# Kernel optimization log

Hardware: AMD Instinct MI355X
Metric: run time of the kernel (lower is better)

Reference implementation:

```python
import jax, jax.numpy as jnp
import numpy as np

D_GNN, D_MODEL = 512, 2048
B, T = 4, 4096
EPS = 1e-5


def layer_norm(x, gamma, beta):
    mu = jnp.mean(x, axis=-1, keepdims=True)
    var = jnp.mean(jnp.square(x - mu), axis=-1, keepdims=True)
    return (x - mu) * jax.lax.rsqrt(var + EPS) * gamma + beta


def setup_inputs() -> dict:
    key = jax.random.key(0)
    ks = jax.random.split(key, 10)
    s_proj = 1.0 / np.sqrt(D_GNN)
    s_mod = 1.0 / np.sqrt(D_MODEL)
    s_gate = 1.0 / np.sqrt(2 * D_MODEL)
    return {
        "h_llm": jax.random.normal(ks[0], (B, T, D_MODEL), jnp.float32),
        "h_change": jax.random.normal(ks[1], (B, D_GNN), jnp.float32),
        # h_change_proj: Linear(d_gnn -> d_model)
        "w_proj": jax.random.uniform(ks[2], (D_MODEL, D_GNN), jnp.float32, -s_proj, s_proj),
        "b_proj": jnp.zeros((D_MODEL,), jnp.float32),
        "g1": jnp.ones((D_MODEL,), jnp.float32),
        "b1": jnp.zeros((D_MODEL,), jnp.float32),
        # MHA value / output projections (q,k are mathematically irrelevant: kv_len==1 -> softmax==1)
        "w_v": jax.random.uniform(ks[3], (D_MODEL, D_MODEL), jnp.float32, -s_mod, s_mod),
        "b_v": jnp.zeros((D_MODEL,), jnp.float32),
        "w_o": jax.random.uniform(ks[4], (D_MODEL, D_MODEL), jnp.float32, -s_mod, s_mod),
        "b_o": jnp.zeros((D_MODEL,), jnp.float32),
        "g2": jnp.ones((D_MODEL,), jnp.float32),
        "b2": jnp.zeros((D_MODEL,), jnp.float32),
        # fusion gate: Linear(2*d_model -> d_model) + sigmoid
        "w_gate": jax.random.uniform(ks[5], (D_MODEL, 2 * D_MODEL), jnp.float32, -s_gate, s_gate),
        "b_gate": jnp.zeros((D_MODEL,), jnp.float32),
        "g3": jnp.ones((D_MODEL,), jnp.float32),
        "b3": jnp.zeros((D_MODEL,), jnp.float32),
    }


def reference(h_llm, h_change, w_proj, b_proj, g1, b1, w_v, b_v, w_o, b_o,
              g2, b2, w_gate, b_gate, g3, b3):
    # project GNN feature to d_model, then LayerNorm  -> (B, D)
    hc = layer_norm(h_change @ w_proj.T + b_proj, g1, b1)
    # cross-attention with kv_len == 1: softmax over a single key is identically 1,
    # so attn_output == out_proj(value_proj(hc)), broadcast over T. Dropout is eval (identity).
    attn = (hc @ w_v.T + b_v) @ w_o.T + b_o                 # (B, D)
    attn_out = layer_norm(h_llm + attn[:, None, :], g2, b2)  # (B, T, D)
    # gated residual fusion: gate = sigmoid(W [h_llm ; attn_out] + b)
    wg_l, wg_a = w_gate[:, :D_MODEL], w_gate[:, D_MODEL:]
    gate = jax.nn.sigmoid(h_llm @ wg_l.T + attn_out @ wg_a.T + b_gate)
    fused = gate * attn_out + (1.0 - gate) * h_llm
    return layer_norm(fused, g3, b3)
```

## Files before the change

kernel.cpp:

```cpp
#include <hip/hip_runtime.h>
#include <hip/hip_bf16.h>
#include <cstdint>
#include <cstddef>

#define DM 2048
#define DG 512
#define NBATCH 4
#define NT 4096
#define NM (NBATCH*NT)
#define KC (2*DM)
#define LN_EPS 1e-5f
#define NTILES (KC/128)
#define SCL_A 16.0f
#define SCL_B 8192.0f
#define DESCALE (1.0f/131072.0f)

typedef __bf16 bf16;
typedef bf16 bf16x8 __attribute__((ext_vector_type(8)));
typedef float f32x4 __attribute__((ext_vector_type(4)));
typedef int   i32x4 __attribute__((ext_vector_type(4)));
typedef char  i8x8  __attribute__((ext_vector_type(8)));

#define AS1 __attribute__((address_space(1)))
#define AS3 __attribute__((address_space(3)))

__device__ __forceinline__ char q8(float x, float s) {
    int v = (int)rintf(x * s);
    v = v > 127 ? 127 : (v < -127 ? -127 : v);
    return (char)v;
}

__device__ __forceinline__ void block_reduce_2(float& s, float& s2) {
#pragma unroll
    for (int off = 32; off; off >>= 1) {
        s  += __shfl_down(s, off);
        s2 += __shfl_down(s2, off);
    }
    __shared__ float sm[8];
    const int wid = threadIdx.x >> 6, lane = threadIdx.x & 63;
    if (lane == 0) { sm[wid] = s; sm[4 + wid] = s2; }
    __syncthreads();
    s  = sm[0] + sm[1] + sm[2] + sm[3];
    s2 = sm[4] + sm[5] + sm[6] + sm[7];
}

__global__ void k_cvt_i8(const float* __restrict__ src, int8_t* __restrict__ dst, int n8) {
    int i = blockIdx.x * blockDim.x + threadIdx.x;
    if (i >= n8) return;
    const f32x4* s = (const f32x4*)src + (size_t)i * 2;
    f32x4 a = s[0], b = s[1];
    i8x8 o;
#pragma unroll
    for (int q = 0; q < 4; q++) { o[q] = q8(a[q], SCL_B); o[4+q] = q8(b[q], SCL_B); }
    *((i8x8*)dst + i) = o;
}

template<int K>
__global__ void k_dot(const float* __restrict__ X, const float* __restrict__ W,
                      const float* __restrict__ bias, float* __restrict__ out) {
    const int lane = threadIdx.x & 63;
    const int wid  = threadIdx.x >> 6;
    const int j = blockIdx.x * 4 + wid;
    const f32x4* Wr = (const f32x4*)(W + (size_t)j * K);
    float acc[NBATCH] = {0.f, 0.f, 0.f, 0.f};
    constexpr int C = K / 4 / 64;
#pragma unroll
    for (int i = 0; i < C; i++) {
        f32x4 wv = Wr[lane + 64 * i];
#pragma unroll
        for (int b = 0; b < NBATCH; b++) {
            f32x4 xv = ((const f32x4*)(X + (size_t)b * K))[lane + 64 * i];
            acc[b] += wv[0]*xv[0] + wv[1]*xv[1] + wv[2]*xv[2] + wv[3]*xv[3];
        }
    }
#pragma unroll
    for (int off = 32; off; off >>= 1)
#pragma unroll
        for (int b = 0; b < NBATCH; b++) acc[b] += __shfl_down(acc[b], off);
    if (lane == 0) {
        const float bb = bias[j];
#pragma unroll
        for (int b = 0; b < NBATCH; b++) out[(size_t)b * DM + j] = acc[b] + bb;
    }
}

__global__ void k_ln_small(const float* __restrict__ in, const float* __restrict__ g,
                           const float* __restrict__ bt, float* __restrict__ out) {
    const int row = blockIdx.x;
    const int tid = threadIdx.x;
    const f32x4* ir = (const f32x4*)(in + (size_t)row * DM);
    f32x4 v0 = ir[tid], v1 = ir[tid + 256];
    float s  = v0[0]+v0[1]+v0[2]+v0[3] + v1[0]+v1[1]+v1[2]+v1[3];
    float s2 = v0[0]*v0[0]+v0[1]*v0[1]+v0[2]*v0[2]+v0[3]*v0[3]
             + v1[0]*v1[0]+v1[1]*v1[1]+v1[2]*v1[2]+v1[3]*v1[3];
    block_reduce_2(s, s2);
    const float mu = s * (1.0f / DM);
    const float r  = rsqrtf(s2 * (1.0f / DM) - mu * mu + LN_EPS);
    f32x4 g0 = ((const f32x4*)g)[tid],  g1v = ((const f32x4*)g)[tid + 256];
    f32x4 b0 = ((const f32x4*)bt)[tid], b1v = ((const f32x4*)bt)[tid + 256];
    f32x4 o0 = (v0 - mu) * r * g0 + b0;
    f32x4 o1 = (v1 - mu) * r * g1v + b1v;
    f32x4* orow = (f32x4*)(out + (size_t)row * DM);
    orow[tid] = o0; orow[tid + 256] = o1;
}

__global__ void k_stats_pack(const float* __restrict__ h, const float* __restrict__ attnv,
                             const float* __restrict__ g2, const float* __restrict__ b2,
                             int8_t* __restrict__ Aq, bf16* __restrict__ hbf,
                             float* __restrict__ muA, float* __restrict__ rA) {
    const int m = blockIdx.x;
    const int b = m >> 12;
    const int tid = threadIdx.x;
    const f32x4* hr = (const f32x4*)(h + (size_t)m * DM);
    const f32x4* ar = (const f32x4*)(attnv + (size_t)b * DM);
    f32x4 h0 = hr[2*tid], h1 = hr[2*tid + 1];
    f32x4 a0 = ar[2*tid], a1 = ar[2*tid + 1];
    f32x4 x0 = h0 + a0, x1 = h1 + a1;
    float s  = x0[0]+x0[1]+x0[2]+x0[3] + x1[0]+x1[1]+x1[2]+x1[3];
    float s2 = x0[0]*x0[0]+x0[1]*x0[1]+x0[2]*x0[2]+x0[3]*x0[3]
             + x1[0]*x1[0]+x1[1]*x1[1]+x1[2]*x1[2]+x1[3]*x1[3];
    block_reduce_2(s, s2);
    const float mu = s * (1.0f / DM);
    const float r  = rsqrtf(s2 * (1.0f / DM) - mu * mu + LN_EPS);
    if (tid == 0) { muA[m] = mu; rA[m] = r; }
    f32x4 gg0 = ((const f32x4*)g2)[2*tid], gg1 = ((const f32x4*)g2)[2*tid + 1];
    f32x4 bb0 = ((const f32x4*)b2)[2*tid], bb1 = ((const f32x4*)b2)[2*tid + 1];
    f32x4 ao0 = (x0 - mu) * r * gg0 + bb0;
    f32x4 ao1 = (x1 - mu) * r * gg1 + bb1;
    bf16x8 hv;
#pragma unroll
    for (int q = 0; q < 4; q++) { hv[q] = (bf16)h0[q]; hv[4+q] = (bf16)h1[q]; }
    *(bf16x8*)(hbf + (size_t)m * DM + 8*tid) = hv;
    i8x8 qh, qa;
#pragma unroll
    for (int q = 0; q < 4; q++) {
        qh[q] = q8(h0[q], SCL_A);  qh[4+q] = q8(h1[q], SCL_A);
        qa[q] = q8(ao0[q], SCL_A); qa[4+q] = q8(ao1[q], SCL_A);
    }
    *(i8x8*)(Aq + (size_t)m * KC + 8*tid) = qh;
    *(i8x8*)(Aq + (size_t)m * KC + DM + 8*tid) = qa;
}

#define MF(a,b,c) __builtin_amdgcn_mfma_i32_16x16x64_i8(a,b,c,0,0,0)
#define SCHED0() __builtin_amdgcn_sched_barrier(0)
#define BAR()  { SCHED0(); asm volatile("s_barrier" ::: "memory"); SCHED0(); }
#define VM(n)  { asm volatile("s_waitcnt vmcnt(" #n ")" ::: "memory"); SCHED0(); }
#define LGKM(n) { asm volatile("s_waitcnt lgkmcnt(" #n ")" ::: "memory"); SCHED0(); }

__global__ __launch_bounds__(512, 2) void k_gemm256(const int8_t* __restrict__ A, const int8_t* __restrict__ Bw,
                                                    const float* __restrict__ bgate, bf16* __restrict__ gl) {
    __shared__ __align__(128) char smem[131072];
    const int tid  = threadIdx.x;
    const int lane = tid & 63;
    const int wid  = tid >> 6;
    const int wm   = wid >> 2, wn = wid & 3;

    const int swz = (blockIdx.x & 7) * 64 + (blockIdx.x >> 3);
    const int bm = (swz >> 3) << 8;
    const int bn = (swz & 7) << 8;

    const int r_local = tid >> 3;
    const int sc = (tid & 7) ^ (r_local & 7);
    const int8_t* Abase = A  + (size_t)(bm + r_local) * KC + sc*16;
    const int8_t* Bbase = Bw + (size_t)(bn + r_local) * KC + sc*16;
    const int ldsW = wid << 10;

#define STAGEA(buf, rnd, kt) __builtin_amdgcn_global_load_lds( \
        (const AS1 void*)(Abase + (size_t)(rnd)*64*KC + (kt)*128), \
        (AS3 void*)(smem + (buf)*65536 + (rnd)*8192 + ldsW), 16, 0, 0)
#define STAGEB(buf, rnd, kt) __builtin_amdgcn_global_load_lds( \
        (const AS1 void*)(Bbase + (size_t)(rnd)*64*KC + (kt)*128), \
        (AS3 void*)(smem + (buf)*65536 + 32768 + (rnd)*8192 + ldsW), 16, 0, 0)

    const int co0 = ((lane >> 4) ^ (lane & 7)) << 4;
    const int co1 = ((4 + (lane >> 4)) ^ (lane & 7)) << 4;
    const int arowb = (wm*128 + (lane & 15)) * 128;
    const int browb = (wn*64  + (lane & 15)) * 128;

#define AFRG(buf, m, ks) (*(const i32x4*)(smem + (buf)*65536 + arowb + (m)*2048 + ((ks) ? co1 : co0)))
#define BFRG(buf, n, ks) (*(const i32x4*)(smem + (buf)*65536 + 32768 + browb + (n)*2048 + ((ks) ? co1 : co0)))

    i32x4 acc[8][4] = {};
    i32x4 aLo[4][2], aHi[4][2], b01[2][2], b23[2][2];

#define LOAD_ALO(buf) { _Pragma("unroll") for (int i = 0; i < 4; i++) { aLo[i][0] = AFRG(buf,i,0);   aLo[i][1] = AFRG(buf,i,1);   } }
#define LOAD_AHI(buf) { _Pragma("unroll") for (int i = 0; i < 4; i++) { aHi[i][0] = AFRG(buf,4+i,0); aHi[i][1] = AFRG(buf,4+i,1); } }
#define LOAD_B01(buf) { _Pragma("unroll") for (int j = 0; j < 2; j++) { b01[j][0] = BFRG(buf,j,0);   b01[j][1] = BFRG(buf,j,1);   } }
#define LOAD_B23(buf) { _Pragma("unroll") for (int j = 0; j < 2; j++) { b23[j][0] = BFRG(buf,2+j,0); b23[j][1] = BFRG(buf,2+j,1); } }

#define MMQ(MOFF, AF, BF, NOFF) { _Pragma("unroll") for (int i = 0; i < 4; i++) \
        _Pragma("unroll") for (int j = 0; j < 2; j++) { \
            acc[(MOFF)+i][(NOFF)+j] = MF(AF[i][0], BF[j][0], acc[(MOFF)+i][(NOFF)+j]); \
            acc[(MOFF)+i][(NOFF)+j] = MF(AF[i][1], BF[j][1], acc[(MOFF)+i][(NOFF)+j]); } }

    STAGEB(0,0,0); STAGEB(0,1,0); STAGEB(0,2,0); STAGEB(0,3,0);
    STAGEA(0,0,0); STAGEA(0,2,0); STAGEA(0,1,0); STAGEA(0,3,0);
    VM(2);
    BAR();

#define TILE_BODY(TT, BUF, NBUF) { \
    const bool g = (TT) < NTILES - 1; \
     \
    if (g) { STAGEB(NBUF,0,(TT)+1); STAGEB(NBUF,1,(TT)+1); } \
    LOAD_ALO(BUF); LOAD_B01(BUF); LOAD_B23(BUF); SCHED0(); \
    LGKM(4); \
    __builtin_amdgcn_s_setprio(1); \
    MMQ(0, aLo, b01, 0); \
    __builtin_amdgcn_s_setprio(0); SCHED0(); \
     \
    if (g) { VM(2); } else { VM(0); } \
    BAR(); \
    if (g) { STAGEB(NBUF,2,(TT)+1); STAGEB(NBUF,3,(TT)+1); } \
    LOAD_AHI(BUF); SCHED0(); \
    LGKM(8); \
    __builtin_amdgcn_s_setprio(1); \
    MMQ(0, aLo, b23, 2); \
    __builtin_amdgcn_s_setprio(0); SCHED0(); \
    BAR(); \
     \
    if (g) { STAGEA(NBUF,0,(TT)+1); STAGEA(NBUF,2,(TT)+1); } \
    LGKM(0); \
    __builtin_amdgcn_s_setprio(1); \
    MMQ(4, aHi, b23, 2); \
    __builtin_amdgcn_s_setprio(0); SCHED0(); \
    BAR(); \
     \
    if (g) { STAGEA(NBUF,1,(TT)+1); STAGEA(NBUF,3,(TT)+1); } \
    __builtin_amdgcn_s_setprio(1); \
    MMQ(4, aHi, b01, 0); \
    __builtin_amdgcn_s_setprio(0); SCHED0(); \
    if (g) { VM(2); } \
    BAR(); \
}

    for (int T = 0; T < NTILES; T += 2) {
        TILE_BODY(T,   0, 1);
        TILE_BODY(T+1, 1, 0);
    }

#pragma unroll
    for (int n = 0; n < 4; n++) {
        const int col = bn + wn*64 + n*16 + (lane & 15);
        const float bg = bgate[col];
#pragma unroll
        for (int m = 0; m < 8; m++) {
            const int row = bm + wm*128 + m*16 + ((lane >> 4) << 2);
#pragma unroll
            for (int r = 0; r < 4; r++)
                gl[(size_t)(row + r) * DM + col] = (bf16)((float)acc[m][n][r] * DESCALE + bg);
        }
    }
}

__global__ void k_epilogue(const bf16* __restrict__ hbf, const bf16* __restrict__ gl,
                           const float* __restrict__ attnv, const float* __restrict__ muA,
                           const float* __restrict__ rA,
                           const float* __restrict__ g2, const float* __restrict__ b2,
                           const float* __restrict__ g3, const float* __restrict__ b3,
                           float* __restrict__ out) {
    const int m = blockIdx.x;
    const int b = m >> 12;
    const int tid = threadIdx.x;
    bf16x8 hb = *(const bf16x8*)(hbf + (size_t)m * DM + 8*tid);
    f32x4 h0, h1;
#pragma unroll
    for (int q = 0; q < 4; q++) { h0[q] = (float)hb[q]; h1[q] = (float)hb[4+q]; }
    const f32x4* ar = (const f32x4*)(attnv + (size_t)b * DM);
    f32x4 a0 = ar[2*tid], a1 = ar[2*tid + 1];
    const float mu = muA[m];
    const float r  = rA[m];
    f32x4 gg0 = ((const f32x4*)g2)[2*tid], gg1 = ((const f32x4*)g2)[2*tid + 1];
    f32x4 bb0 = ((const f32x4*)b2)[2*tid], bb1 = ((const f32x4*)b2)[2*tid + 1];
    f32x4 ao0 = (h0 + a0 - mu) * r * gg0 + bb0;
    f32x4 ao1 = (h1 + a1 - mu) * r * gg1 + bb1;
    bf16x8 qv = *(const bf16x8*)(gl + (size_t)m * DM + 8*tid);
    f32x4 gt0, gt1;
#pragma unroll
    for (int q = 0; q < 4; q++) {
        gt0[q] = 1.0f / (1.0f + __expf(-(float)qv[q]));
        gt1[q] = 1.0f / (1.0f + __expf(-(float)qv[4+q]));
    }
    f32x4 f0 = h0 + gt0 * (ao0 - h0);
    f32x4 f1 = h1 + gt1 * (ao1 - h1);
    float s  = f0[0]+f0[1]+f0[2]+f0[3] + f1[0]+f1[1]+f1[2]+f1[3];
    float s2 = f0[0]*f0[0]+f0[1]*f0[1]+f0[2]*f0[2]+f0[3]*f0[3]
             + f1[0]*f1[0]+f1[1]*f1[1]+f1[2]*f1[2]+f1[3]*f1[3];
    block_reduce_2(s, s2);
    const float mu3 = s * (1.0f / DM);
    const float r3  = rsqrtf(s2 * (1.0f / DM) - mu3 * mu3 + LN_EPS);
    f32x4 g30 = ((const f32x4*)g3)[2*tid], g31 = ((const f32x4*)g3)[2*tid + 1];
    f32x4 b30 = ((const f32x4*)b3)[2*tid], b31 = ((const f32x4*)b3)[2*tid + 1];
    f32x4 o0 = (f0 - mu3) * r3 * g30 + b30;
    f32x4 o1 = (f1 - mu3) * r3 * g31 + b31;
    f32x4* orow = (f32x4*)(out + (size_t)m * DM);
    orow[2*tid] = o0; orow[2*tid + 1] = o1;
}

extern "C" void kernel_launch(void* const* d_in, const int* in_sizes, int n_in,
                              void* d_out, int out_size, void* d_ws, size_t ws_size,
                              hipStream_t stream) {
    const float* h_llm    = (const float*)d_in[0];
    const float* h_change = (const float*)d_in[1];
    const float* w_proj   = (const float*)d_in[2];
    const float* b_proj   = (const float*)d_in[3];
    const float* g1       = (const float*)d_in[4];
    const float* b1       = (const float*)d_in[5];
    const float* w_v      = (const float*)d_in[6];
    const float* b_v      = (const float*)d_in[7];
    const float* w_o      = (const float*)d_in[8];
    const float* b_o      = (const float*)d_in[9];
    const float* g2       = (const float*)d_in[10];
    const float* b2       = (const float*)d_in[11];
    const float* w_gate   = (const float*)d_in[12];
    const float* b_gate   = (const float*)d_in[13];
    const float* g3       = (const float*)d_in[14];
    const float* b3       = (const float*)d_in[15];
    float* out = (float*)d_out;

    char* ws = (char*)d_ws;
    int8_t* Aq  = (int8_t*)ws; ws += (size_t)NM * KC;
    int8_t* wqb = (int8_t*)ws; ws += (size_t)DM * KC;
    bf16* hbf = (bf16*)ws;    ws += (size_t)NM * DM * 2;
    bf16* gl  = (bf16*)ws;    ws += (size_t)NM * DM * 2;
    float* muA = (float*)ws;  ws += (size_t)NM * 4;
    float* rA  = (float*)ws;  ws += (size_t)NM * 4;
    float* raw1 = (float*)ws; ws += (size_t)NBATCH * DM * 4;
    float* hc   = (float*)ws; ws += (size_t)NBATCH * DM * 4;
    float* raw2 = (float*)ws; ws += (size_t)NBATCH * DM * 4;
    float* attnv= (float*)ws; ws += (size_t)NBATCH * DM * 4;

    k_cvt_i8<<<(DM * KC / 8 + 255) / 256, 256, 0, stream>>>(w_gate, wqb, DM * KC / 8);
    k_dot<DG><<<DM / 4, 256, 0, stream>>>(h_change, w_proj, b_proj, raw1);
    k_ln_small<<<NBATCH, 256, 0, stream>>>(raw1, g1, b1, hc);
    k_dot<DM><<<DM / 4, 256, 0, stream>>>(hc, w_v, b_v, raw2);
    k_dot<DM><<<DM / 4, 256, 0, stream>>>(raw2, w_o, b_o, attnv);
    k_stats_pack<<<NM, 256, 0, stream>>>(h_llm, attnv, g2, b2, Aq, hbf, muA, rA);
    k_gemm256<<<512, 512, 0, stream>>>(Aq, wqb, b_gate, gl);
    k_epilogue<<<NM, 256, 0, stream>>>(hbf, gl, attnv, muA, rA, g2, b2, g3, b3, out);
}
```

Measured before the change: 290.4 us.

## Fold sigmoid into GEMM epilogue, store gate as u8, simplify staging pipeline

Result: faster. 279.6 us (-3.7%).

```diff
diff --git a/kernel.cpp b/kernel.cpp
--- a/kernel.cpp
+++ b/kernel.cpp
@@ -20,6 +20,7 @@
 typedef float f32x4 __attribute__((ext_vector_type(4)));
 typedef int   i32x4 __attribute__((ext_vector_type(4)));
 typedef char  i8x8  __attribute__((ext_vector_type(8)));
+typedef unsigned char u8x8 __attribute__((ext_vector_type(8)));
 
 #define AS1 __attribute__((address_space(1)))
 #define AS3 __attribute__((address_space(3)))
@@ -148,7 +149,7 @@
 #define LGKM(n) { asm volatile("s_waitcnt lgkmcnt(" #n ")" ::: "memory"); SCHED0(); }
 
 __global__ __launch_bounds__(512, 2) void k_gemm256(const int8_t* __restrict__ A, const int8_t* __restrict__ Bw,
-                                                    const float* __restrict__ bgate, bf16* __restrict__ gl) {
+                                                    const float* __restrict__ bgate, uint8_t* __restrict__ gq) {
     __shared__ __align__(128) char smem[131072];
     const int tid  = threadIdx.x;
     const int lane = tid & 63;
@@ -195,41 +196,35 @@
 
     STAGEB(0,0,0); STAGEB(0,1,0); STAGEB(0,2,0); STAGEB(0,3,0);
     STAGEA(0,0,0); STAGEA(0,2,0); STAGEA(0,1,0); STAGEA(0,3,0);
-    VM(2);
+    VM(0);
     BAR();
 
 #define TILE_BODY(TT, BUF, NBUF) { \
     const bool g = (TT) < NTILES - 1; \
      \
-    if (g) { STAGEB(NBUF,0,(TT)+1); STAGEB(NBUF,1,(TT)+1); } \
+    if (g) { STAGEB(NBUF,0,(TT)+1); STAGEB(NBUF,1,(TT)+1); STAGEB(NBUF,2,(TT)+1); STAGEB(NBUF,3,(TT)+1); } \
     LOAD_ALO(BUF); LOAD_B01(BUF); LOAD_B23(BUF); SCHED0(); \
     LGKM(4); \
     __builtin_amdgcn_s_setprio(1); \
     MMQ(0, aLo, b01, 0); \
     __builtin_amdgcn_s_setprio(0); SCHED0(); \
      \
-    if (g) { VM(2); } else { VM(0); } \
-    BAR(); \
-    if (g) { STAGEB(NBUF,2,(TT)+1); STAGEB(NBUF,3,(TT)+1); } \
+    if (g) { STAGEA(NBUF,0,(TT)+1); STAGEA(NBUF,1,(TT)+1); STAGEA(NBUF,2,(TT)+1); STAGEA(NBUF,3,(TT)+1); } \
     LOAD_AHI(BUF); SCHED0(); \
     LGKM(8); \
     __builtin_amdgcn_s_setprio(1); \
     MMQ(0, aLo, b23, 2); \
     __builtin_amdgcn_s_setprio(0); SCHED0(); \
-    BAR(); \
      \
-    if (g) { STAGEA(NBUF,0,(TT)+1); STAGEA(NBUF,2,(TT)+1); } \
     LGKM(0); \
     __builtin_amdgcn_s_setprio(1); \
     MMQ(4, aHi, b23, 2); \
     __builtin_amdgcn_s_setprio(0); SCHED0(); \
-    BAR(); \
      \
-    if (g) { STAGEA(NBUF,1,(TT)+1); STAGEA(NBUF,3,(TT)+1); } \
     __builtin_amdgcn_s_setprio(1); \
     MMQ(4, aHi, b01, 0); \
     __builtin_amdgcn_s_setprio(0); SCHED0(); \
-    if (g) { VM(2); } \
+    VM(0); \
     BAR(); \
 }
 
@@ -246,13 +241,16 @@
         for (int m = 0; m < 8; m++) {
             const int row = bm + wm*128 + m*16 + ((lane >> 4) << 2);
 #pragma unroll
-            for (int r = 0; r < 4; r++)
-                gl[(size_t)(row + r) * DM + col] = (bf16)((float)acc[m][n][r] * DESCALE + bg);
+            for (int r = 0; r < 4; r++) {
+                const float z = (float)acc[m][n][r] * DESCALE + bg;
+                const float gate = 1.0f / (1.0f + __expf(-z));
+                gq[(size_t)(row + r) * DM + col] = (uint8_t)(int)rintf(gate * 255.0f);
+            }
         }
     }
 }
 
-__global__ void k_epilogue(const bf16* __restrict__ hbf, const bf16* __restrict__ gl,
+__global__ void k_epilogue(const bf16* __restrict__ hbf, const uint8_t* __restrict__ gq,
                            const float* __restrict__ attnv, const float* __restrict__ muA,
                            const float* __restrict__ rA,
                            const float* __restrict__ g2, const float* __restrict__ b2,
@@ -273,12 +271,12 @@
     f32x4 bb0 = ((const f32x4*)b2)[2*tid], bb1 = ((const f32x4*)b2)[2*tid + 1];
     f32x4 ao0 = (h0 + a0 - mu) * r * gg0 + bb0;
     f32x4 ao1 = (h1 + a1 - mu) * r * gg1 + bb1;
-    bf16x8 qv = *(const bf16x8*)(gl + (size_t)m * DM + 8*tid);
+    u8x8 qv = *(const u8x8*)(gq + (size_t)m * DM + 8*tid);
     f32x4 gt0, gt1;
 #pragma unroll
     for (int q = 0; q < 4; q++) {
-        gt0[q] = 1.0f / (1.0f + __expf(-(float)qv[q]));
-        gt1[q] = 1.0f / (1.0f + __expf(-(float)qv[4+q]));
+        gt0[q] = (float)qv[q]   * (1.0f / 255.0f);
+        gt1[q] = (float)qv[4+q] * (1.0f / 255.0f);
     }
     f32x4 f0 = h0 + gt0 * (ao0 - h0);
     f32x4 f1 = h1 + gt1 * (ao1 - h1);
@@ -321,7 +319,7 @@
     int8_t* Aq  = (int8_t*)ws; ws += (size_t)NM * KC;
     int8_t* wqb = (int8_t*)ws; ws += (size_t)DM * KC;
     bf16* hbf = (bf16*)ws;    ws += (size_t)NM * DM * 2;
-    bf16* gl  = (bf16*)ws;    ws += (size_t)NM * DM * 2;
+    uint8_t* gq = (uint8_t*)ws; ws += (size_t)NM * DM;
     float* muA = (float*)ws;  ws += (size_t)NM * 4;
     float* rA  = (float*)ws;  ws += (size_t)NM * 4;
     float* raw1 = (float*)ws; ws += (size_t)NBATCH * DM * 4;
@@ -335,6 +333,6 @@
     k_dot<DM><<<DM / 4, 256, 0, stream>>>(hc, w_v, b_v, raw2);
     k_dot<DM><<<DM / 4, 256, 0, stream>>>(raw2, w_o, b_o, attnv);
     k_stats_pack<<<NM, 256, 0, stream>>>(h_llm, attnv, g2, b2, Aq, hbf, muA, rA);
-    k_gemm256<<<512, 512, 0, stream>>>(Aq, wqb, b_gate, gl);
-    k_epilogue<<<NM, 256, 0, stream>>>(hbf, gl, attnv, muA, rA, g2, b2, g3, b3, out);
-}
+    k_gemm256<<<512, 512, 0, stream>>>(Aq, wqb, b_gate, gq);
+    k_epilogue<<<NM, 256, 0, stream>>>(hbf, gq, attnv, muA, rA, g2, b2, g3, b3, out);
+}
```
